# Kernel tuning notes

Hardware: AMD Instinct MI355X
Metric: run time of the kernel (lower is better)

Reference implementation:

```python
import jax, jax.numpy as jnp
import numpy as np

# Granite-8B-like dims
B, S, H = 4, 1024, 4096
NH, NKV, D = 32, 8, 128          # query heads, kv heads (GQA), head_dim
PG, NPAGES = 128, 64             # page_size, pool size
PPS = S // PG                    # pages per sequence = 8
SCALE = 0.08838834764831845      # attention_multiplier (1/sqrt(128))
SOFTCAP = 50.0                   # attention_logit_softcapping


def rotate_half(x):
    x1, x2 = jnp.split(x, 2, axis=-1)
    return jnp.concatenate([-x2, x1], axis=-1)


def setup_inputs() -> dict:
    key = jax.random.key(0)
    ks = jax.random.split(key, 5)
    hidden_states = jax.random.normal(ks[0], (B, S, H), jnp.float32)
    wq = jax.random.normal(ks[1], (H, NH * D), jnp.float32) * 0.02
    wk = jax.random.normal(ks[2], (H, NKV * D), jnp.float32) * 0.02
    wv = jax.random.normal(ks[3], (H, NKV * D), jnp.float32) * 0.02
    wo = jax.random.normal(ks[4], (NH * D, H), jnp.float32) * 0.02
    # RoPE tables (HF convention), position_ids = arange(S)
    inv_freq = 1.0 / (10000.0 ** (jnp.arange(0, D, 2, dtype=jnp.float32) / D))
    freqs = jnp.outer(jnp.arange(S, dtype=jnp.float32), inv_freq)  # [S, D/2]
    emb = jnp.concatenate([freqs, freqs], axis=-1)                 # [S, D]
    cos, sin = jnp.cos(emb), jnp.sin(emb)
    # Disjoint random physical pages per sequence (page-table indirection)
    perm = np.random.default_rng(0).permutation(NPAGES)[: B * PPS]
    page_table = jnp.asarray(perm.reshape(B, PPS), jnp.int32)      # [B, PPS]
    return dict(hidden_states=hidden_states, wq=wq, wk=wk, wv=wv, wo=wo,
                cos=cos, sin=sin, page_table=page_table)


def reference(hidden_states, wq, wk, wv, wo, cos, sin, page_table):
    Bb, Ss, _ = hidden_states.shape
    # projections + head split: [B, nH, S, D]
    q = (hidden_states @ wq).reshape(Bb, Ss, NH, D).transpose(0, 2, 1, 3)
    k = (hidden_states @ wk).reshape(Bb, Ss, NKV, D).transpose(0, 2, 1, 3)
    v = (hidden_states @ wv).reshape(Bb, Ss, NKV, D).transpose(0, 2, 1, 3)
    # RoPE (cos/sin broadcast over batch and heads)
    q = q * cos + rotate_half(q) * sin
    k = k * cos + rotate_half(k) * sin
    # physical slot for each (b, s): page_table[b, s//PG]*PG + s%PG
    s_idx = jnp.arange(Ss)
    phys = page_table[:, s_idx // PG] * PG + (s_idx % PG)           # [B, S]
    N = NPAGES * PG
    # scatter K/V into the shared paged cache (pages are disjoint across B)
    k_flat = k.transpose(1, 0, 2, 3).reshape(NKV, Bb * Ss, D)
    v_flat = v.transpose(1, 0, 2, 3).reshape(NKV, Bb * Ss, D)
    flat = phys.reshape(-1)
    k_cache = jnp.zeros((NKV, N, D), hidden_states.dtype).at[:, flat, :].set(k_flat)
    v_cache = jnp.zeros((NKV, N, D), hidden_states.dtype).at[:, flat, :].set(v_flat)
    # gather back in logical order per sequence: [B, NKV, S, D]
    k_log = k_cache[:, phys, :].transpose(1, 0, 2, 3)
    v_log = v_cache[:, phys, :].transpose(1, 0, 2, 3)
    # GQA: expand kv heads to query heads
    g = NH // NKV
    kr = jnp.repeat(k_log, g, axis=1)
    vr = jnp.repeat(v_log, g, axis=1)
    # scaled QK -> softcap -> causal mask (score_mod order) -> softmax
    scores = jnp.einsum('bhqd,bhkd->bhqk', q, kr) * SCALE
    scores = SOFTCAP * jnp.tanh(scores / SOFTCAP)
    causal = jnp.tril(jnp.ones((Ss, Ss), bool))
    scores = jnp.where(causal, scores, jnp.finfo(scores.dtype).min)
    p = jax.nn.softmax(scores, axis=-1)
    out = jnp.einsum('bhqk,bhkd->bhqd', p, vr)
    out = out.transpose(0, 2, 1, 3).reshape(Bb, Ss, NH * D)
    return out @ wo
```

## Files before the change

### kernel.cpp

```cpp
#include <hip/hip_runtime.h>
#include <hip/hip_bf16.h>


#define S_    1024
#define NQKV  6144
#define SCALE_   0.08838834764831845f
#define SOFTCAP_ 50.0f

typedef __bf16 bf16x8 __attribute__((ext_vector_type(8)));
typedef float  f32x4  __attribute__((ext_vector_type(4)));
typedef unsigned int  u32;
typedef unsigned short u16;

static __device__ __forceinline__ u16 f2bf(float f) {
  union { float f; u32 u; } v; v.f = f;
  u32 u = v.u;
  u32 r = u + 0x7FFFu + ((u >> 16) & 1u);
  return (u16)(r >> 16);
}
static __device__ __forceinline__ float bf2f(u16 s) {
  union { u32 u; float f; } v; v.u = ((u32)s) << 16; return v.f;
}

static __device__ __forceinline__ void gload_lds16(const void* g, void* l) {
  __builtin_amdgcn_global_load_lds(
      (const __attribute__((address_space(1))) void*)g,
      (__attribute__((address_space(3))) void*)l, 16, 0, 0);
}

__global__ __launch_bounds__(256) void cast_bf16(const float* __restrict__ X,
                                                 u16* __restrict__ Y) {
  size_t i = (size_t)blockIdx.x * 256 + threadIdx.x;
  float4 a = ((const float4*)X)[2 * i];
  float4 b = ((const float4*)X)[2 * i + 1];
  union { u16 h[8]; f32x4 v; } o;
  o.h[0] = f2bf(a.x); o.h[1] = f2bf(a.y); o.h[2] = f2bf(a.z); o.h[3] = f2bf(a.w);
  o.h[4] = f2bf(b.x); o.h[5] = f2bf(b.y); o.h[6] = f2bf(b.z); o.h[7] = f2bf(b.w);
  ((f32x4*)Y)[i] = o.v;
}

__global__ __launch_bounds__(256) void transpose_w(const float* __restrict__ W,
                                                   u16* __restrict__ WT, int N) {
  __shared__ float t[32][33];
  const int K = 4096;
  int n0 = blockIdx.x * 32, k0 = blockIdx.y * 32;
  int tx = threadIdx.x & 31, ty = threadIdx.x >> 5;
#pragma unroll
  for (int j = 0; j < 4; ++j)
    t[ty + 8 * j][tx] = W[(size_t)(k0 + ty + 8 * j) * N + n0 + tx];
  __syncthreads();
#pragma unroll
  for (int j = 0; j < 4; ++j)
    WT[(size_t)(n0 + ty + 8 * j) * K + k0 + tx] = f2bf(t[tx][ty + 8 * j]);
}

template <bool OUT_BF16>
__global__ __launch_bounds__(256) void gemm_mfma(const u16* __restrict__ A,
                                                 const u16* __restrict__ Bt,
                                                 void* __restrict__ Cp,
                                                 int N, int K) {
  __shared__ u16 As[128 * 32];
  __shared__ u16 Bs[128 * 32];
  int tid = threadIdx.x;
  int wave = tid >> 6, lane = tid & 63;
  int quad = lane >> 4, l16 = lane & 15;
  int wrow = (wave >> 1) * 64, wcol = (wave & 1) * 64;
  int m0 = blockIdx.y * 128, n0 = blockIdx.x * 128;

  f32x4 acc[4][4];
#pragma unroll
  for (int i = 0; i < 4; ++i)
#pragma unroll
    for (int j = 0; j < 4; ++j)
#pragma unroll
      for (int c = 0; c < 4; ++c) acc[i][j][c] = 0.0f;

  int lr = lane >> 2, lc = lane & 3;
  const u16* ga = A  + (size_t)(m0 + wave * 32 + lr) * K + lc * 8;
  const u16* gb = Bt + (size_t)(n0 + wave * 32 + lr) * K + lc * 8;
  u16* lA0 = &As[(wave * 32) * 32];
  u16* lA1 = &As[(wave * 32 + 16) * 32];
  u16* lB0 = &Bs[(wave * 32) * 32];
  u16* lB1 = &Bs[(wave * 32 + 16) * 32];
  const size_t rstep = (size_t)16 * K;

  for (int k0 = 0; k0 < K; k0 += 32) {
    gload_lds16(ga + k0,         lA0);
    gload_lds16(ga + rstep + k0, lA1);
    gload_lds16(gb + k0,         lB0);
    gload_lds16(gb + rstep + k0, lB1);
    __syncthreads();
    bf16x8 af[4], bfr[4];
#pragma unroll
    for (int fi = 0; fi < 4; ++fi) {
      af[fi]  = *(const bf16x8*)&As[(wrow + fi * 16 + l16) * 32 + quad * 8];
      bfr[fi] = *(const bf16x8*)&Bs[(wcol + fi * 16 + l16) * 32 + quad * 8];
    }
#pragma unroll
    for (int mf = 0; mf < 4; ++mf)
#pragma unroll
      for (int nf = 0; nf < 4; ++nf)
        acc[mf][nf] = __builtin_amdgcn_mfma_f32_16x16x32_bf16(
            af[mf], bfr[nf], acc[mf][nf], 0, 0, 0);
    __syncthreads();
  }
#pragma unroll
  for (int mf = 0; mf < 4; ++mf)
#pragma unroll
    for (int nf = 0; nf < 4; ++nf)
#pragma unroll
      for (int r = 0; r < 4; ++r) {
        int row = m0 + wrow + mf * 16 + quad * 4 + r;
        int col = n0 + wcol + nf * 16 + l16;
        float v = acc[mf][nf][r];
        if (OUT_BF16) ((u16*)Cp)[(size_t)row * N + col] = f2bf(v);
        else          ((float*)Cp)[(size_t)row * N + col] = v;
      }
}

__global__ __launch_bounds__(256) void rope_kernel(u16* __restrict__ QKV,
                                                   const float* __restrict__ cosT,
                                                   const float* __restrict__ sinT) {
  int row = blockIdx.x;
  int s = row & (S_ - 1);
  size_t base = (size_t)row * NQKV;
#pragma unroll
  for (int i = 0; i < 10; ++i) {
    int e = threadIdx.x + 256 * i;
    int head = e >> 6, d = e & 63;
    int col = head * 128 + d;
    float c = cosT[s * 128 + d];
    float sn = sinT[s * 128 + d];
    float x1 = bf2f(QKV[base + col]);
    float x2 = bf2f(QKV[base + col + 64]);
    QKV[base + col]      = f2bf(x1 * c - x2 * sn);
    QKV[base + col + 64] = f2bf(x2 * c + x1 * sn);
  }
}

__global__ __launch_bounds__(256) void attn_kernel(const u16* __restrict__ QKV,
                                                   u16* __restrict__ ctx) {
  __shared__ __align__(16) u16 ks[64 * 128];
  __shared__ __align__(16) u16 vT[128 * 72];
  __shared__ __align__(16) u16 ps[4][16 * 72];
  int bx = blockIdx.x;
  int qt = bx & 15, h = (bx >> 4) & 31, b = bx >> 9;
  int kvh = h >> 2;
  int tid = threadIdx.x, wave = tid >> 6, lane = tid & 63;
  int quad = lane >> 4, l16 = lane & 15;
  int q0 = qt * 64 + wave * 16;

  bf16x8 qf[4];
  {
    const u16* qrow = QKV + (size_t)(b * S_ + q0 + l16) * NQKV + h * 128;
#pragma unroll
    for (int k4 = 0; k4 < 4; ++k4)
      qf[k4] = *(const bf16x8*)(qrow + k4 * 32 + quad * 8);
  }
  f32x4 acc[8];
#pragma unroll
  for (int i = 0; i < 8; ++i)
#pragma unroll
    for (int r = 0; r < 4; ++r) acc[i][r] = 0.0f;
  float m[4], l[4];
#pragma unroll
  for (int r = 0; r < 4; ++r) { m[r] = -3e30f; l[r] = 0.f; }

  const u16* kbase = QKV + (size_t)(b * S_) * NQKV + 4096 + kvh * 128;
  const u32* vbase = (const u32*)(QKV + (size_t)(b * S_) * NQKV + 5120 + kvh * 128);

  for (int c = 0; c <= qt; ++c) {
    __syncthreads();
#pragma unroll
    for (int i = 0; i < 4; ++i) {
      int e = tid + 256 * i;
      int kr = e >> 4, c16 = e & 15;
      f32x4 kv = *(const f32x4*)(kbase + (size_t)(c * 64 + kr) * NQKV + c16 * 8);
      u32 off = (u32)(kr * 256 + c16 * 16) ^ (u32)((kr & 7) << 4);
      *(f32x4*)((char*)ks + off) = kv;
    }
    {
      int klo = lane & 1, A = (lane >> 1) & 3, D = (lane >> 3) & 7;
#pragma unroll
      for (int i = 0; i < 16; ++i) {
        int ti = wave * 16 + i;
        int kb = ti >> 3, db = ti & 7;
        int key = kb * 8 + 2 * A + klo, dp = db * 8 + D;
        u32 v  = vbase[(size_t)(c * 64 + key) * (NQKV / 2) + dp];
        u32 vo = __shfl_xor(v, 1, 64);
        u32 w = klo ? ((vo >> 16) | (v & 0xFFFF0000u))
                    : ((v & 0xFFFFu) | (vo << 16));
        int d = 2 * dp + klo;
        int kp = kb * 4 + A;
        *(u32*)((char*)vT + d * 144 + kp * 4) = w;
      }
    }
    __syncthreads();

    f32x4 s[4];
#pragma unroll
    for (int nf = 0; nf < 4; ++nf) {
#pragma unroll
      for (int r = 0; r < 4; ++r) s[nf][r] = 0.0f;
      int row = l16 + 16 * nf;
#pragma unroll
      for (int k4 = 0; k4 < 4; ++k4) {
        u32 off = (u32)(row * 256 + k4 * 64 + quad * 16) ^ (u32)((row & 7) << 4);
        bf16x8 kf = *(const bf16x8*)((const char*)ks + off);
        s[nf] = __builtin_amdgcn_mfma_f32_16x16x32_bf16(qf[k4], kf, s[nf], 0, 0, 0);
      }
    }
#pragma unroll
    for (int r = 0; r < 4; ++r) {
      float sc[4];
#pragma unroll
      for (int nf = 0; nf < 4; ++nf) {
        float x = s[nf][r] * SCALE_;
        float e2 = __expf(x * (2.0f / SOFTCAP_));
        sc[nf] = SOFTCAP_ * (1.0f - 2.0f / (e2 + 1.0f));
      }
      if (c == qt) {
        int row = wave * 16 + quad * 4 + r;
#pragma unroll
        for (int nf = 0; nf < 4; ++nf)
          if (nf * 16 + l16 > row) sc[nf] = -1e30f;
      }
      float cm = fmaxf(fmaxf(sc[0], sc[1]), fmaxf(sc[2], sc[3]));
#pragma unroll
      for (int off = 8; off >= 1; off >>= 1)
        cm = fmaxf(cm, __shfl_xor(cm, off, 64));
      float mn = fmaxf(m[r], cm);
      float alpha = __expf(m[r] - mn);
      float p[4], psum = 0.f;
#pragma unroll
      for (int nf = 0; nf < 4; ++nf) { p[nf] = __expf(sc[nf] - mn); psum += p[nf]; }
#pragma unroll
      for (int off = 8; off >= 1; off >>= 1) psum += __shfl_xor(psum, off, 64);
      l[r] = l[r] * alpha + psum;
      m[r] = mn;
#pragma unroll
      for (int i = 0; i < 8; ++i) acc[i][r] *= alpha;
#pragma unroll
      for (int nf = 0; nf < 4; ++nf)
        ps[wave][(quad * 4 + r) * 72 + nf * 16 + l16] = f2bf(p[nf]);
    }
    bf16x8 pa[2];
#pragma unroll
    for (int k2 = 0; k2 < 2; ++k2)
      pa[k2] = *(const bf16x8*)&ps[wave][l16 * 72 + k2 * 32 + quad * 8];
#pragma unroll
    for (int nf = 0; nf < 8; ++nf) {
      int d = l16 + 16 * nf;
#pragma unroll
      for (int k2 = 0; k2 < 2; ++k2) {
        bf16x8 vf = *(const bf16x8*)((const char*)vT + d * 144 + k2 * 64 + quad * 16);
        acc[nf] = __builtin_amdgcn_mfma_f32_16x16x32_bf16(pa[k2], vf, acc[nf], 0, 0, 0);
      }
    }
  }
#pragma unroll
  for (int r = 0; r < 4; ++r) {
    float inv = 1.0f / l[r];
    size_t rowoff = (size_t)(b * S_ + q0 + quad * 4 + r) * 4096 + h * 128;
#pragma unroll
    for (int nf = 0; nf < 8; ++nf)
      ctx[rowoff + nf * 16 + l16] = f2bf(acc[nf][r] * inv);
  }
}

extern "C" void kernel_launch(void* const* d_in, const int* in_sizes, int n_in,
                              void* d_out, int out_size, void* d_ws, size_t ws_size,
                              hipStream_t stream) {
  (void)in_sizes; (void)n_in; (void)out_size; (void)ws_size;
  const float* hidden = (const float*)d_in[0];
  const float* wq = (const float*)d_in[1];
  const float* wk = (const float*)d_in[2];
  const float* wv = (const float*)d_in[3];
  const float* wo = (const float*)d_in[4];
  const float* cosT = (const float*)d_in[5];
  const float* sinT = (const float*)d_in[6];

  u16* WT  = (u16*)d_ws;
  u16* QKV = WT + (size_t)10240 * 4096;
  u16* CTX = WT;
  u16* Hbf = (u16*)d_out;

  transpose_w<<<dim3(4096 / 32, 128), 256, 0, stream>>>(wq, WT, 4096);
  transpose_w<<<dim3(1024 / 32, 128), 256, 0, stream>>>(wk, WT + (size_t)4096 * 4096, 1024);
  transpose_w<<<dim3(1024 / 32, 128), 256, 0, stream>>>(wv, WT + (size_t)5120 * 4096, 1024);
  transpose_w<<<dim3(4096 / 32, 128), 256, 0, stream>>>(wo, WT + (size_t)6144 * 4096, 4096);
  cast_bf16<<<8192, 256, 0, stream>>>(hidden, Hbf);

  gemm_mfma<true><<<dim3(6144 / 128, 4096 / 128), 256, 0, stream>>>(
      Hbf, WT, QKV, 6144, 4096);
  rope_kernel<<<4096, 256, 0, stream>>>(QKV, cosT, sinT);
  attn_kernel<<<2048, 256, 0, stream>>>(QKV, CTX);
  gemm_mfma<false><<<dim3(4096 / 128, 4096 / 128), 256, 0, stream>>>(
      CTX, WT + (size_t)6144 * 4096, d_out, 4096, 4096);
}
```

Baseline: 1.079 ms.

## Prefetch next K/V tile into registers, swizzle LDS, vectorize RoPE

The attention loop now issues global loads for the next K/V chunk into registers before computing the current chunk, then writes them to LDS after a barrier, so memory latency overlaps the QK and PV MFMA work. The padded vT and P buffers are replaced with XOR-swizzled unpadded layouts to avoid bank conflicts while using less LDS. s_setprio is raised around the MFMA sections. The RoPE kernel processes two bf16 values per thread with u32 and float2 loads. The cost is extra registers for the prefetched tiles, which may reduce occupancy.

Result: faster. 995.2 us (-7.8%).

```diff
diff --git a/kernel.cpp b/kernel.cpp
--- a/kernel.cpp
+++ b/kernel.cpp
@@ -123,26 +123,31 @@
                                                    const float* __restrict__ sinT) {
   int row = blockIdx.x;
   int s = row & (S_ - 1);
-  size_t base = (size_t)row * NQKV;
-#pragma unroll
-  for (int i = 0; i < 10; ++i) {
+  u32* Q32 = (u32*)(QKV + (size_t)row * NQKV);
+  const float2* c2 = (const float2*)(cosT + s * 128);
+  const float2* s2 = (const float2*)(sinT + s * 128);
+#pragma unroll
+  for (int i = 0; i < 5; ++i) {
     int e = threadIdx.x + 256 * i;
-    int head = e >> 6, d = e & 63;
-    int col = head * 128 + d;
-    float c = cosT[s * 128 + d];
-    float sn = sinT[s * 128 + d];
-    float x1 = bf2f(QKV[base + col]);
-    float x2 = bf2f(QKV[base + col + 64]);
-    QKV[base + col]      = f2bf(x1 * c - x2 * sn);
-    QKV[base + col + 64] = f2bf(x2 * c + x1 * sn);
+    int head = e >> 5, dd = e & 31;
+    int col2 = head * 64 + dd;
+    u32 a = Q32[col2];
+    u32 b = Q32[col2 + 32];
+    float2 c = c2[dd], sn = s2[dd];
+    float x1a = bf2f((u16)a), x1b = bf2f((u16)(a >> 16));
+    float x2a = bf2f((u16)b), x2b = bf2f((u16)(b >> 16));
+    Q32[col2]      = (u32)f2bf(x1a * c.x - x2a * sn.x) |
+                     ((u32)f2bf(x1b * c.y - x2b * sn.y) << 16);
+    Q32[col2 + 32] = (u32)f2bf(x2a * c.x + x1a * sn.x) |
+                     ((u32)f2bf(x2b * c.y + x1b * sn.y) << 16);
   }
 }
 
 __global__ __launch_bounds__(256) void attn_kernel(const u16* __restrict__ QKV,
                                                    u16* __restrict__ ctx) {
   __shared__ __align__(16) u16 ks[64 * 128];
-  __shared__ __align__(16) u16 vT[128 * 72];
-  __shared__ __align__(16) u16 ps[4][16 * 72];
+  __shared__ __align__(16) u16 vT[128 * 64];
+  __shared__ __align__(16) u16 ps[4][16 * 64];
   int bx = blockIdx.x;
   int qt = bx & 15, h = (bx >> 4) & 31, b = bx >> 9;
   int kvh = h >> 2;
@@ -169,35 +174,59 @@
   const u16* kbase = QKV + (size_t)(b * S_) * NQKV + 4096 + kvh * 128;
   const u32* vbase = (const u32*)(QKV + (size_t)(b * S_) * NQKV + 5120 + kvh * 128);
 
+  int krow = tid >> 4, kc16 = tid & 15;
+  int klo = lane & 1, A = (lane >> 1) & 3, D = (lane >> 3) & 7;
+  int vkey0 = 2 * A + klo;
+
+  f32x4 kreg[4];
+  u32 vreg[16];
+
+  auto LOADK = [&](int cc) {
+#pragma unroll
+    for (int i = 0; i < 4; ++i)
+      kreg[i] = *(const f32x4*)(kbase +
+                 (size_t)(cc * 64 + krow + 16 * i) * NQKV + kc16 * 8);
+  };
+  auto LOADV = [&](int cc) {
+#pragma unroll
+    for (int i = 0; i < 16; ++i) {
+      int key = (wave * 2 + (i >> 3)) * 8 + vkey0;
+      int dp  = (i & 7) * 8 + D;
+      vreg[i] = vbase[(size_t)(cc * 64 + key) * (NQKV / 2) + dp];
+    }
+  };
+  auto WRITEK = [&]() {
+#pragma unroll
+    for (int i = 0; i < 4; ++i) {
+      int r = krow + 16 * i;
+      u32 off = (u32)(r * 256 + kc16 * 16) ^ (u32)((r & 7) << 4);
+      *(f32x4*)((char*)ks + off) = kreg[i];
+    }
+  };
+  auto WRITEV = [&]() {
+#pragma unroll
+    for (int i = 0; i < 16; ++i) {
+      u32 v = vreg[i];
+      u32 vo = __shfl_xor(v, 1, 64);
+      u32 w = klo ? ((vo >> 16) | (v & 0xFFFF0000u))
+                  : ((v & 0xFFFFu) | (vo << 16));
+      int dp = (i & 7) * 8 + D;
+      int d = 2 * dp + klo;
+      int kp = (wave * 2 + (i >> 3)) * 4 + A;
+      u32 off = (u32)(d * 128 + kp * 4) ^ (u32)((d & 7) << 4);
+      *(u32*)((char*)vT + off) = w;
+    }
+  };
+
+  LOADK(0); LOADV(0);
+  WRITEK(); WRITEV();
+  __syncthreads();
+
   for (int c = 0; c <= qt; ++c) {
-    __syncthreads();
-#pragma unroll
-    for (int i = 0; i < 4; ++i) {
-      int e = tid + 256 * i;
-      int kr = e >> 4, c16 = e & 15;
-      f32x4 kv = *(const f32x4*)(kbase + (size_t)(c * 64 + kr) * NQKV + c16 * 8);
-      u32 off = (u32)(kr * 256 + c16 * 16) ^ (u32)((kr & 7) << 4);
-      *(f32x4*)((char*)ks + off) = kv;
-    }
-    {
-      int klo = lane & 1, A = (lane >> 1) & 3, D = (lane >> 3) & 7;
-#pragma unroll
-      for (int i = 0; i < 16; ++i) {
-        int ti = wave * 16 + i;
-        int kb = ti >> 3, db = ti & 7;
-        int key = kb * 8 + 2 * A + klo, dp = db * 8 + D;
-        u32 v  = vbase[(size_t)(c * 64 + key) * (NQKV / 2) + dp];
-        u32 vo = __shfl_xor(v, 1, 64);
-        u32 w = klo ? ((vo >> 16) | (v & 0xFFFF0000u))
-                    : ((v & 0xFFFFu) | (vo << 16));
-        int d = 2 * dp + klo;
-        int kp = kb * 4 + A;
-        *(u32*)((char*)vT + d * 144 + kp * 4) = w;
-      }
-    }
-    __syncthreads();
+    if (c < qt) { LOADK(c + 1); LOADV(c + 1); }
 
     f32x4 s[4];
+    __builtin_amdgcn_s_setprio(1);
 #pragma unroll
     for (int nf = 0; nf < 4; ++nf) {
 #pragma unroll
@@ -210,6 +239,8 @@
         s[nf] = __builtin_amdgcn_mfma_f32_16x16x32_bf16(qf[k4], kf, s[nf], 0, 0, 0);
       }
     }
+    __builtin_amdgcn_s_setprio(0);
+
 #pragma unroll
     for (int r = 0; r < 4; ++r) {
       float sc[4];
@@ -240,22 +271,36 @@
       m[r] = mn;
 #pragma unroll
       for (int i = 0; i < 8; ++i) acc[i][r] *= alpha;
-#pragma unroll
-      for (int nf = 0; nf < 4; ++nf)
-        ps[wave][(quad * 4 + r) * 72 + nf * 16 + l16] = f2bf(p[nf]);
+      int prow = quad * 4 + r;
+#pragma unroll
+      for (int nf = 0; nf < 4; ++nf) {
+        u32 off = (u32)(prow * 128 + (nf * 16 + l16) * 2) ^ (u32)((prow & 7) << 4);
+        *(u16*)((char*)&ps[wave][0] + off) = f2bf(p[nf]);
+      }
     }
     bf16x8 pa[2];
 #pragma unroll
-    for (int k2 = 0; k2 < 2; ++k2)
-      pa[k2] = *(const bf16x8*)&ps[wave][l16 * 72 + k2 * 32 + quad * 8];
+    for (int k2 = 0; k2 < 2; ++k2) {
+      u32 off = (u32)(l16 * 128 + k2 * 64 + quad * 16) ^ (u32)((l16 & 7) << 4);
+      pa[k2] = *(const bf16x8*)((const char*)&ps[wave][0] + off);
+    }
+    __builtin_amdgcn_s_setprio(1);
 #pragma unroll
     for (int nf = 0; nf < 8; ++nf) {
       int d = l16 + 16 * nf;
 #pragma unroll
       for (int k2 = 0; k2 < 2; ++k2) {
-        bf16x8 vf = *(const bf16x8*)((const char*)vT + d * 144 + k2 * 64 + quad * 16);
+        u32 off = (u32)(d * 128 + k2 * 64 + quad * 16) ^ (u32)((d & 7) << 4);
+        bf16x8 vf = *(const bf16x8*)((const char*)vT + off);
         acc[nf] = __builtin_amdgcn_mfma_f32_16x16x32_bf16(pa[k2], vf, acc[nf], 0, 0, 0);
       }
+    }
+    __builtin_amdgcn_s_setprio(0);
+
+    __syncthreads();
+    if (c < qt) {
+      WRITEK(); WRITEV();
+      __syncthreads();
     }
   }
 #pragma unroll
```
